# Kernel optimization log

Hardware: AMD Instinct MI355X
Metric: run time of the kernel (lower is better)

The kernel has to match this reference:

```python
import jax, jax.numpy as jnp
import numpy as np

H = 16       # num_attention_heads
KV = 4       # num_key_value_heads
HD = 128     # head_dim
BASE = 10000.0


def rotate_half(x):
    x1, x2 = jnp.split(x, 2, axis=-1)
    return jnp.concatenate((-x2, x1), axis=-1)


def rope_cos_sin(position_ids):
    # inv_freq: (HD/2,)
    inv_freq = 1.0 / (BASE ** (jnp.arange(0, HD, 2, dtype=jnp.float32) / HD))
    freqs = position_ids.astype(jnp.float32)[..., None] * inv_freq  # (B, S, HD/2)
    emb = jnp.concatenate((freqs, freqs), axis=-1)  # (B, S, HD)
    return jnp.cos(emb), jnp.sin(emb)


def setup_inputs() -> dict:
    key = jax.random.key(0)
    ks = jax.random.split(key, 5)
    B, S, D = 2, 2048, 2048
    sc = 1.0 / np.sqrt(D)
    return {
        "hidden_states": jax.random.normal(ks[0], (B, S, D), jnp.float32),
        "position_ids": jnp.broadcast_to(jnp.arange(S, dtype=jnp.int32), (B, S)),
        "wq": jax.random.normal(ks[1], (H * HD, D), jnp.float32) * sc,
        "wk": jax.random.normal(ks[2], (KV * HD, D), jnp.float32) * sc,
        "wv": jax.random.normal(ks[3], (KV * HD, D), jnp.float32) * sc,
        "wo": jax.random.normal(ks[4], (H * HD, H * HD), jnp.float32) * sc,
    }


def attention_forward(hidden_states, position_ids, wq, wk, wv, wo):
    B, S, D = hidden_states.shape
    n_rep = H // KV
    # projections -> (B, heads, S, HD)
    q = (hidden_states @ wq.T).reshape(B, S, H, HD).transpose(0, 2, 1, 3)
    k = (hidden_states @ wk.T).reshape(B, S, KV, HD).transpose(0, 2, 1, 3)
    v = (hidden_states @ wv.T).reshape(B, S, KV, HD).transpose(0, 2, 1, 3)
    # RoPE
    cos, sin = rope_cos_sin(position_ids)  # (B, S, HD)
    cos = cos[:, None]  # (B, 1, S, HD)
    sin = sin[:, None]
    q = q * cos + rotate_half(q) * sin
    k = k * cos + rotate_half(k) * sin
    # repeat kv heads for GQA: (B, KV, S, HD) -> (B, H, S, HD)
    k = jnp.repeat(k, n_rep, axis=1)
    v = jnp.repeat(v, n_rep, axis=1)
    scale = 1.0 / np.sqrt(HD)
    scores = jnp.einsum("bhqd,bhkd->bhqk", q, k) * scale
    attn = jax.nn.softmax(scores.astype(jnp.float32), axis=-1).astype(q.dtype)
    out = jnp.einsum("bhqk,bhkd->bhqd", attn, v)
    out = out.transpose(0, 2, 1, 3).reshape(B, S, H * HD)
    return out @ wo.T


def reference(hidden_states, position_ids, wq, wk, wv, wo):
    return attention_forward(hidden_states, position_ids, wq, wk, wv, wo)
```

## Files before the change

kernel.cpp:

```cpp
#include <hip/hip_runtime.h>
#include <hip/hip_bf16.h>
#include <math.h>


typedef __attribute__((ext_vector_type(4))) float f32x4;
typedef __attribute__((ext_vector_type(8))) short short8;
typedef __attribute__((ext_vector_type(4))) unsigned short u16x4;
typedef __attribute__((ext_vector_type(8))) unsigned short u16x8;

static __device__ __forceinline__ unsigned short f2bf(float x) {
    unsigned u = __builtin_bit_cast(unsigned, x);
    u += 0x7fffu + ((u >> 16) & 1u);
    return (unsigned short)(u >> 16);
}
static __device__ __forceinline__ float bf2f(unsigned short h) {
    unsigned u = ((unsigned)h) << 16;
    return __builtin_bit_cast(float, u);
}
static __device__ __forceinline__ float exp2_fast(float x) {
    float r;
    asm volatile("v_exp_f32 %0, %1" : "=v"(r) : "v"(x));
    return r;
}
static __device__ __forceinline__ void gload16(const unsigned short* g, unsigned short* lds) {
    __builtin_amdgcn_global_load_lds((const __attribute__((address_space(1))) void*)g,
                                     (__attribute__((address_space(3))) void*)lds, 16, 0, 0);
}

__global__ __launch_bounds__(256) void k_prep(const float* __restrict__ hs,
                                              const float* __restrict__ wq,
                                              const float* __restrict__ wk,
                                              const float* __restrict__ wv,
                                              const float* __restrict__ wo,
                                              const int* __restrict__ pos_ids,
                                              unsigned short* __restrict__ hsb,
                                              unsigned short* __restrict__ wqkvb,
                                              unsigned short* __restrict__ wob,
                                              float2* __restrict__ tb) {
    long idx = (long)blockIdx.x * 256 + threadIdx.x;
    if (idx < 2097152) {
        f32x4 v = ((const f32x4*)hs)[idx];
        u16x4 o;
        o.x = f2bf(v.x); o.y = f2bf(v.y); o.z = f2bf(v.z); o.w = f2bf(v.w);
        ((u16x4*)hsb)[idx] = o;
    } else if (idx < 3670016) {
        long i = idx - 2097152;
        long flat = i * 4;
        int row = (int)(flat >> 11);
        int col = (int)(flat & 2047);
        const float* src;
        if (row < 2560) {
            int base = row & 2047;
            int hh = base >> 7, ii = base & 127;
            int d = (ii >> 1) + ((ii & 1) << 6);
            src = (row < 2048 ? wq : wk) + (size_t)(hh * 128 + d) * 2048;
        } else {
            src = wv + (size_t)(row - 2560) * 2048;
        }
        f32x4 v = *(const f32x4*)(src + col);
        u16x4 o;
        o.x = f2bf(v.x); o.y = f2bf(v.y); o.z = f2bf(v.z); o.w = f2bf(v.w);
        *(u16x4*)(wqkvb + flat) = o;
    } else if (idx < 4718592) {
        long i = idx - 3670016;
        f32x4 v = ((const f32x4*)wo)[i];
        u16x4 o;
        o.x = f2bf(v.x); o.y = f2bf(v.y); o.z = f2bf(v.z); o.w = f2bf(v.w);
        ((u16x4*)wob)[i] = o;
    } else {
        long j = idx - 4718592;
        int r = (int)(j >> 6);
        int i = (int)(j & 63);
        float pos = (float)pos_ids[r];
        float powv = (float)pow(10000.0, (double)i / 64.0);
        float invf = 1.0f / powv;
        float arg  = pos * invf;
        double a = (double)arg;
        tb[(size_t)r * 64 + i] = make_float2((float)cos(a), (float)sin(a));
    }
}

template <int EPI>
__global__ __launch_bounds__(256) void k_gemm(const unsigned short* __restrict__ A,
                                              const unsigned short* __restrict__ W,
                                              float* __restrict__ Cf,
                                              unsigned short* __restrict__ qkvt,
                                              unsigned short* __restrict__ vtb,
                                              const float2* __restrict__ tb,
                                              int M, int N, int K) {
    __shared__ unsigned short As[2][4096];
    __shared__ unsigned short Ws[2][4096];
    const int tid = threadIdx.x;
    const int lane = tid & 63;
    const int w = tid >> 6;
    const int q = lane & 15, g = lane >> 4;
    const int wr = w >> 1, wc = w & 1;

    const int nwg = gridDim.x * gridDim.y;
    const int id = blockIdx.y * gridDim.x + blockIdx.x;
    const int swz_id = (id & 7) * (nwg >> 3) + (id >> 3);
    const int bx = swz_id % gridDim.x;
    const int by = swz_id / gridDim.x;
    const long mbase = (long)by * 128;
    const long nbase = (long)bx * 128;

    const unsigned short* gA[2];
    const unsigned short* gW[2];
    #pragma unroll
    for (int j = 0; j < 2; ++j) {
        int r = j * 64 + (tid >> 2);
        int slot = (tid & 3) ^ ((r >> 1) & 3);
        gA[j] = A + (size_t)(mbase + r) * K + slot * 8;
        gW[j] = W + (size_t)(nbase + r) * K + slot * 8;
    }
    const int sa = (g ^ ((q >> 1) & 3)) * 8;

    f32x4 acc[4][4];
    #pragma unroll
    for (int m = 0; m < 4; ++m)
        #pragma unroll
        for (int n = 0; n < 4; ++n) acc[m][n] = (f32x4){0.f, 0.f, 0.f, 0.f};

    auto STAGE = [&](int buf) {
        #pragma unroll
        for (int j = 0; j < 2; ++j) {
            gload16(gA[j], &As[buf][j * 2048 + w * 512]);
            gload16(gW[j], &Ws[buf][j * 2048 + w * 512]);
            gA[j] += 32; gW[j] += 32;
        }
    };

    const int nk = K >> 5;
    STAGE(0);
    int cur = 0;
    for (int t = 0; t < nk; ++t) {
        if (t) __builtin_amdgcn_s_barrier();
        if (t + 1 < nk) {
            STAGE(cur ^ 1);
            asm volatile("s_waitcnt vmcnt(4)" ::: "memory");
        } else {
            asm volatile("s_waitcnt vmcnt(0)" ::: "memory");
        }
        __builtin_amdgcn_s_barrier();

        short8 af[4], bfr[4];
        #pragma unroll
        for (int m = 0; m < 4; ++m) af[m] = *(const short8*)&As[cur][(wr * 64 + m * 16 + q) * 32 + sa];
        #pragma unroll
        for (int n = 0; n < 4; ++n) bfr[n] = *(const short8*)&Ws[cur][(wc * 64 + n * 16 + q) * 32 + sa];
        #pragma unroll
        for (int m = 0; m < 4; ++m)
            #pragma unroll
            for (int n = 0; n < 4; ++n)
                acc[m][n] = __builtin_amdgcn_mfma_f32_16x16x32_bf16(af[m], bfr[n], acc[m][n], 0, 0, 0);
        cur ^= 1;
    }

    if (EPI == 0) {
        #pragma unroll
        for (int m = 0; m < 4; ++m)
            #pragma unroll
            for (int n = 0; n < 4; ++n)
                #pragma unroll
                for (int rr = 0; rr < 4; ++rr) {
                    long row = mbase + wr * 64 + m * 16 + 4 * g + rr;
                    long col = nbase + wc * 64 + n * 16 + q;
                    Cf[row * N + col] = acc[m][n][rr];
                }
    } else {
        const int tile = bx;
        if (tile >= 20) {
            const int kv = tile - 20;
            #pragma unroll
            for (int m = 0; m < 4; ++m)
                #pragma unroll
                for (int n = 0; n < 4; ++n) {
                    int c = wc * 64 + n * 16 + q;
                    long r0 = mbase + wr * 64 + m * 16 + 4 * g;
                    int b = (int)(r0 >> 11), s0 = (int)(r0 & 2047);
                    u16x4 pk;
                    #pragma unroll
                    for (int rr = 0; rr < 4; ++rr) pk[rr] = f2bf(acc[m][n][rr]);
                    *(u16x4*)(vtb + (size_t)((b * 4 + kv) * 128 + c) * 2048 + s0) = pk;
                }
        } else {
            const float scale = (tile < 16) ? 0.12751744f : 1.0f;
            const float sgn = (q & 1) ? 1.f : -1.f;
            #pragma unroll
            for (int m = 0; m < 4; ++m)
                #pragma unroll
                for (int rr = 0; rr < 4; ++rr) {
                    long row = mbase + wr * 64 + m * 16 + 4 * g + rr;
                    #pragma unroll
                    for (int n = 0; n < 4; ++n) {
                        int c = wc * 64 + n * 16 + q;
                        float x = acc[m][n][rr];
                        float p = __shfl_xor(x, 1);
                        float2 cs = tb[row * 64 + (c >> 1)];
                        float y = (x * cs.x + sgn * (p * cs.y)) * scale;
                        int dorig = (c >> 1) + ((c & 1) << 6);
                        long col = (tile < 16) ? (tile * 128 + dorig)
                                               : (2048 + (tile - 16) * 128 + dorig);
                        qkvt[row * 3072 + col] = f2bf(y);
                    }
                }
        }
    }
}

__global__ __launch_bounds__(256, 2) void k_flash(const unsigned short* __restrict__ qkv,
                                                  const unsigned short* __restrict__ vt,
                                                  unsigned short* __restrict__ aout) {
    __shared__ unsigned short Ks[2][8192];
    __shared__ unsigned short Vs[2][8192];
    __shared__ unsigned short Plds[4][1152];
    const int wg = blockIdx.x;
    const int kvg = wg & 7;
    const int inner = wg >> 3;
    const int h_in = inner & 3;
    const int qt = inner >> 2;
    const int b = kvg >> 2, kvh = kvg & 3;
    const int h = kvh * 4 + h_in;
    const int tid = threadIdx.x;
    const int w = tid >> 6, lane = tid & 63;
    const int q = lane & 15, g = lane >> 4;
    const int qrow = qt * 128 + w * 32;

    short8 qf[2][4];
    #pragma unroll
    for (int u = 0; u < 2; ++u) {
        const unsigned short* Qp = qkv + (size_t)(b * 2048 + qrow + u * 16 + q) * 3072 + h * 128 + g * 8;
        #pragma unroll
        for (int t = 0; t < 4; ++t) qf[u][t] = *(const short8*)(Qp + t * 32);
    }

    const unsigned short* Kbase = qkv + (size_t)(b * 2048) * 3072 + 2048 + kvh * 128;
    const unsigned short* Vbase = vt + (size_t)((b * 4 + kvh) * 128) * 2048;
    const unsigned short* gK[4];
    const unsigned short* gV[4];
    #pragma unroll
    for (int i = 0; i < 4; ++i) {
        int rowK = w * 16 + i * 4 + (lane >> 4);
        gK[i] = Kbase + (size_t)rowK * 3072 + (((lane & 15) ^ (rowK & 7)) << 3);
        int rowV = w * 32 + i * 8 + (lane >> 3);
        gV[i] = Vbase + (size_t)rowV * 2048 + (((lane & 7) ^ (rowV & 7)) << 3);
    }

    const int swz = (q & 7) << 3;
    int tcK[4];
    #pragma unroll
    for (int t = 0; t < 4; ++t) tcK[t] = (t * 32 + g * 8) ^ swz;

    unsigned short* Pw = Plds[w];

    float m_run[2] = {-INFINITY, -INFINITY};
    float l_run[2] = {0.f, 0.f};
    f32x4 o[2][8];
    #pragma unroll
    for (int u = 0; u < 2; ++u)
        #pragma unroll
        for (int nf = 0; nf < 8; ++nf) o[u][nf] = (f32x4){0.f, 0.f, 0.f, 0.f};

    auto STAGE = [&](int buf) {
        #pragma unroll
        for (int i = 0; i < 4; ++i) {
            gload16(gK[i], &Ks[buf][w * 2048 + i * 512]);
            gload16(gV[i], &Vs[buf][w * 2048 + i * 512]);
            gK[i] += 64 * 3072;
            gV[i] += 64;
        }
    };

    STAGE(0);
    int cur = 0;
    for (int t0 = 0; t0 < 32; ++t0) {
        if (t0 > 0) __builtin_amdgcn_s_barrier();
        if (t0 + 1 < 32) {
            STAGE(cur ^ 1);
            asm volatile("s_waitcnt vmcnt(8)" ::: "memory");
        } else {
            asm volatile("s_waitcnt vmcnt(0)" ::: "memory");
        }
        __builtin_amdgcn_s_barrier();

        const unsigned short* Kt = Ks[cur];
        const unsigned short* Vt = Vs[cur];

        f32x4 st[2][4];
        #pragma unroll
        for (int ks = 0; ks < 4; ++ks) {
            f32x4 a0 = (f32x4){0.f, 0.f, 0.f, 0.f};
            f32x4 a1 = (f32x4){0.f, 0.f, 0.f, 0.f};
            int rb = (ks * 16 + q) * 128;
            #pragma unroll
            for (int t = 0; t < 4; ++t) {
                short8 kf = *(const short8*)&Kt[rb + tcK[t]];
                a0 = __builtin_amdgcn_mfma_f32_16x16x32_bf16(kf, qf[0][t], a0, 0, 0, 0);
                a1 = __builtin_amdgcn_mfma_f32_16x16x32_bf16(kf, qf[1][t], a1, 0, 0, 0);
            }
            st[0][ks] = a0; st[1][ks] = a1;
        }

        short8 vf[8][2];
        #pragma unroll
        for (int nf = 0; nf < 8; ++nf) {
            int rb = (nf * 16 + q) * 64;
            #pragma unroll
            for (int t = 0; t < 2; ++t) vf[nf][t] = *(const short8*)&Vt[rb + tcK[t]];
        }

        #pragma unroll
        for (int u = 0; u < 2; ++u) {
            float mx = fmaxf(
                fmaxf(fmaxf(fmaxf(st[u][0][0], st[u][0][1]), fmaxf(st[u][0][2], st[u][0][3])),
                      fmaxf(fmaxf(st[u][1][0], st[u][1][1]), fmaxf(st[u][1][2], st[u][1][3]))),
                fmaxf(fmaxf(fmaxf(st[u][2][0], st[u][2][1]), fmaxf(st[u][2][2], st[u][2][3])),
                      fmaxf(fmaxf(st[u][3][0], st[u][3][1]), fmaxf(st[u][3][2], st[u][3][3]))));
            mx = fmaxf(mx, __shfl_xor(mx, 16));
            mx = fmaxf(mx, __shfl_xor(mx, 32));
            if (__any(mx - m_run[u] > 8.0f)) {
                float mn = fmaxf(m_run[u], mx);
                float sc = exp2_fast(m_run[u] - mn);
                l_run[u] *= sc;
                f32x4 sv;
                #pragma unroll
                for (int rr = 0; rr < 4; ++rr) sv[rr] = __shfl(sc, 4 * g + rr);
                #pragma unroll
                for (int nf = 0; nf < 8; ++nf) o[u][nf] *= sv;
                m_run[u] = mn;
            }
            f32x4 pe[4];
            #pragma unroll
            for (int ks = 0; ks < 4; ++ks)
                #pragma unroll
                for (int rr = 0; rr < 4; ++rr) pe[ks][rr] = exp2_fast(st[u][ks][rr] - m_run[u]);
            f32x4 ls4 = (pe[0] + pe[1]) + (pe[2] + pe[3]);
            float ls = (ls4[0] + ls4[1]) + (ls4[2] + ls4[3]);
            ls += __shfl_xor(ls, 16);
            ls += __shfl_xor(ls, 32);
            l_run[u] += ls;

            #pragma unroll
            for (int ks = 0; ks < 4; ++ks) {
                u16x4 pk;
                #pragma unroll
                for (int rr = 0; rr < 4; ++rr) pk[rr] = f2bf(pe[ks][rr]);
                *(u16x4*)&Pw[q * 72 + ks * 16 + 4 * g] = pk;
            }
            asm volatile("s_waitcnt lgkmcnt(0)" ::: "memory");
            short8 pa0 = *(const short8*)&Pw[q * 72 + g * 8];
            short8 pa1 = *(const short8*)&Pw[q * 72 + 32 + g * 8];

            #pragma unroll
            for (int nf = 0; nf < 8; ++nf) {
                f32x4 a = o[u][nf];
                a = __builtin_amdgcn_mfma_f32_16x16x32_bf16(pa0, vf[nf][0], a, 0, 0, 0);
                a = __builtin_amdgcn_mfma_f32_16x16x32_bf16(pa1, vf[nf][1], a, 0, 0, 0);
                o[u][nf] = a;
            }
        }
        cur ^= 1;
    }

    #pragma unroll
    for (int u = 0; u < 2; ++u) {
        f32x4 li;
        #pragma unroll
        for (int rr = 0; rr < 4; ++rr) li[rr] = __shfl(l_run[u], 4 * g + rr);
        #pragma unroll
        for (int nf = 0; nf < 8; ++nf)
            #pragma unroll
            for (int rr = 0; rr < 4; ++rr) {
                size_t row = (size_t)(b * 2048 + qrow + u * 16 + 4 * g + rr);
                aout[row * 2048 + h * 128 + nf * 16 + q] = f2bf(o[u][nf][rr] / li[rr]);
            }
    }
}

extern "C" void kernel_launch(void* const* d_in, const int* in_sizes, int n_in,
                              void* d_out, int out_size, void* d_ws, size_t ws_size,
                              hipStream_t stream) {
    (void)in_sizes; (void)n_in; (void)out_size; (void)ws_size;
    const float* hs = (const float*)d_in[0];
    const int* pos  = (const int*)d_in[1];
    const float* wq = (const float*)d_in[2];
    const float* wk = (const float*)d_in[3];
    const float* wv = (const float*)d_in[4];
    const float* wo = (const float*)d_in[5];
    float* out = (float*)d_out;

    unsigned short* hsb   = (unsigned short*)d_ws;
    unsigned short* wqkvb = hsb + (size_t)4096 * 2048;
    unsigned short* wob   = wqkvb + (size_t)3072 * 2048;
    unsigned short* qkvt  = wob + (size_t)2048 * 2048;
    unsigned short* vtb   = qkvt + (size_t)4096 * 3072;
    float2* tb            = (float2*)(vtb + (size_t)8 * 128 * 2048);
    unsigned short* aoutb = (unsigned short*)(tb + (size_t)4096 * 64);

    k_prep<<<19456, 256, 0, stream>>>(hs, wq, wk, wv, wo, pos, hsb, wqkvb, wob, tb);
    k_gemm<1><<<dim3(24, 32), 256, 0, stream>>>(hsb, wqkvb, nullptr, qkvt, vtb, tb, 4096, 3072, 2048);
    k_flash<<<dim3(512), 256, 0, stream>>>(qkvt, vtb, aoutb);
    k_gemm<0><<<dim3(16, 32), 256, 0, stream>>>(aoutb, wob, out, nullptr, nullptr, nullptr, 4096, 2048, 2048);
}
```

Before: 226.5 us.

## Rewrite projection GEMMs with 8-wave 256-row tiles and phased K=64 pipelining

Replaces the 128x128, 4-wave GEMM with an 8-wave (512-thread) kernel. The QKV projection now uses 256x256 tiles and the output projection 256x128 tiles, with a K-step of 64 and an XOR-swizzled LDS layout. The main loop is split into phases that interleave global-to-LDS prefetch of the next tile with MFMA work on the current one, and raise wave priority around the MFMA blocks. The aim is more data reuse per LDS load and better overlap of memory with compute. The cost is more barriers, higher register and LDS pressure, and fewer workgroups (192 and 256) on a large-CU GPU, so occupancy and wave quantization may suffer.

```diff
diff --git a/kernel.cpp b/kernel.cpp
--- a/kernel.cpp
+++ b/kernel.cpp
@@ -12,10 +12,6 @@
     unsigned u = __builtin_bit_cast(unsigned, x);
     u += 0x7fffu + ((u >> 16) & 1u);
     return (unsigned short)(u >> 16);
-}
-static __device__ __forceinline__ float bf2f(unsigned short h) {
-    unsigned u = ((unsigned)h) << 16;
-    return __builtin_bit_cast(float, u);
 }
 static __device__ __forceinline__ float exp2_fast(float x) {
     float r;
@@ -81,130 +77,201 @@
 }
 
 template <int EPI>
-__global__ __launch_bounds__(256) void k_gemm(const unsigned short* __restrict__ A,
-                                              const unsigned short* __restrict__ W,
-                                              float* __restrict__ Cf,
-                                              unsigned short* __restrict__ qkvt,
-                                              unsigned short* __restrict__ vtb,
-                                              const float2* __restrict__ tb,
-                                              int M, int N, int K) {
-    __shared__ unsigned short As[2][4096];
-    __shared__ unsigned short Ws[2][4096];
+__global__ __launch_bounds__(512, 2) void k_gemm8(const unsigned short* __restrict__ A,
+                                                  const unsigned short* __restrict__ W,
+                                                  float* __restrict__ Cf,
+                                                  unsigned short* __restrict__ qkvt,
+                                                  unsigned short* __restrict__ vtb,
+                                                  const float2* __restrict__ tb,
+                                                  int M, int N, int K) {
+    constexpr int BN = EPI ? 256 : 128;
+    constexpr int BHALF = BN / 128;
+    __shared__ unsigned short As[2][16384];
+    __shared__ unsigned short Bs[2][BN * 64];
     const int tid = threadIdx.x;
     const int lane = tid & 63;
     const int w = tid >> 6;
     const int q = lane & 15, g = lane >> 4;
-    const int wr = w >> 1, wc = w & 1;
+    const int wr = w >> 2, wc = w & 3;
 
     const int nwg = gridDim.x * gridDim.y;
     const int id = blockIdx.y * gridDim.x + blockIdx.x;
     const int swz_id = (id & 7) * (nwg >> 3) + (id >> 3);
     const int bx = swz_id % gridDim.x;
     const int by = swz_id / gridDim.x;
-    const long mbase = (long)by * 128;
-    const long nbase = (long)bx * 128;
-
-    const unsigned short* gA[2];
-    const unsigned short* gW[2];
-    #pragma unroll
-    for (int j = 0; j < 2; ++j) {
-        int r = j * 64 + (tid >> 2);
-        int slot = (tid & 3) ^ ((r >> 1) & 3);
-        gA[j] = A + (size_t)(mbase + r) * K + slot * 8;
-        gW[j] = W + (size_t)(nbase + r) * K + slot * 8;
-    }
-    const int sa = (g ^ ((q >> 1) & 3)) * 8;
-
-    f32x4 acc[4][4];
-    #pragma unroll
-    for (int m = 0; m < 4; ++m)
-        #pragma unroll
-        for (int n = 0; n < 4; ++n) acc[m][n] = (f32x4){0.f, 0.f, 0.f, 0.f};
-
-    auto STAGE = [&](int buf) {
-        #pragma unroll
-        for (int j = 0; j < 2; ++j) {
-            gload16(gA[j], &As[buf][j * 2048 + w * 512]);
-            gload16(gW[j], &Ws[buf][j * 2048 + w * 512]);
-            gA[j] += 32; gW[j] += 32;
-        }
+    const long mbase = (long)by * 256;
+    const long nbase = (long)bx * BN;
+
+    const int lr = lane >> 3;
+    const int lslot = (lane & 7) ^ lr;
+    const unsigned short* pA[2][2];
+    const unsigned short* pB[BHALF][2];
+    #pragma unroll
+    for (int h = 0; h < 2; ++h)
+        #pragma unroll
+        for (int j = 0; j < 2; ++j)
+            pA[h][j] = A + (size_t)(mbase + h * 128 + w * 16 + j * 8 + lr) * K + lslot * 8;
+    #pragma unroll
+    for (int h = 0; h < BHALF; ++h)
+        #pragma unroll
+        for (int j = 0; j < 2; ++j)
+            pB[h][j] = W + (size_t)(nbase + h * 128 + w * 16 + j * 8 + lr) * K + lslot * 8;
+
+    auto ISSUE_A = [&](int buf, int h) {
+        gload16(pA[h][0], &As[buf][h * 8192 + w * 1024]);
+        gload16(pA[h][1], &As[buf][h * 8192 + w * 1024 + 512]);
+        pA[h][0] += 64; pA[h][1] += 64;
     };
-
-    const int nk = K >> 5;
-    STAGE(0);
-    int cur = 0;
-    for (int t = 0; t < nk; ++t) {
-        if (t) __builtin_amdgcn_s_barrier();
-        if (t + 1 < nk) {
-            STAGE(cur ^ 1);
-            asm volatile("s_waitcnt vmcnt(4)" ::: "memory");
-        } else {
-            asm volatile("s_waitcnt vmcnt(0)" ::: "memory");
-        }
-        __builtin_amdgcn_s_barrier();
-
-        short8 af[4], bfr[4];
-        #pragma unroll
-        for (int m = 0; m < 4; ++m) af[m] = *(const short8*)&As[cur][(wr * 64 + m * 16 + q) * 32 + sa];
-        #pragma unroll
-        for (int n = 0; n < 4; ++n) bfr[n] = *(const short8*)&Ws[cur][(wc * 64 + n * 16 + q) * 32 + sa];
-        #pragma unroll
-        for (int m = 0; m < 4; ++m)
-            #pragma unroll
-            for (int n = 0; n < 4; ++n)
-                acc[m][n] = __builtin_amdgcn_mfma_f32_16x16x32_bf16(af[m], bfr[n], acc[m][n], 0, 0, 0);
-        cur ^= 1;
-    }
-
-    if (EPI == 0) {
-        #pragma unroll
-        for (int m = 0; m < 4; ++m)
-            #pragma unroll
-            for (int n = 0; n < 4; ++n)
-                #pragma unroll
-                for (int rr = 0; rr < 4; ++rr) {
-                    long row = mbase + wr * 64 + m * 16 + 4 * g + rr;
-                    long col = nbase + wc * 64 + n * 16 + q;
-                    Cf[row * N + col] = acc[m][n][rr];
+    auto ISSUE_B = [&](int buf, int h) {
+        gload16(pB[h][0], &Bs[buf][h * 8192 + w * 1024]);
+        gload16(pB[h][1], &Bs[buf][h * 8192 + w * 1024 + 512]);
+        pB[h][0] += 64; pB[h][1] += 64;
+    };
+
+    const int xs = q & 7;
+    const int sl0 = (g ^ xs) * 8;
+    const int sl1 = ((4 + g) ^ xs) * 8;
+
+    const int NT = K >> 6;
+
+    if constexpr (EPI == 1) {
+        f32x4 acc[8][4];
+        #pragma unroll
+        for (int m = 0; m < 8; ++m)
+            #pragma unroll
+            for (int n = 0; n < 4; ++n) acc[m][n] = (f32x4){0.f, 0.f, 0.f, 0.f};
+        short8 a[4][2], bq[2][2];
+
+        auto loadA = [&](int cur, int mh) {
+            #pragma unroll
+            for (int mq = 0; mq < 4; ++mq) {
+                int r = (wr * 128 + mh * 64 + mq * 16 + q) * 64;
+                a[mq][0] = *(const short8*)&As[cur][r + sl0];
+                a[mq][1] = *(const short8*)&As[cur][r + sl1];
+            }
+        };
+        auto loadB = [&](int cur, int nh) {
+            #pragma unroll
+            for (int nq = 0; nq < 2; ++nq) {
+                int r = (wc * 64 + nh * 32 + nq * 16 + q) * 64;
+                bq[nq][0] = *(const short8*)&Bs[cur][r + sl0];
+                bq[nq][1] = *(const short8*)&Bs[cur][r + sl1];
+            }
+        };
+        auto mm = [&](int mh, int nh) {
+            __builtin_amdgcn_s_setprio(1);
+            #pragma unroll
+            for (int mq = 0; mq < 4; ++mq)
+                #pragma unroll
+                for (int nq = 0; nq < 2; ++nq) {
+                    f32x4 c = acc[mh * 4 + mq][nh * 2 + nq];
+                    c = __builtin_amdgcn_mfma_f32_16x16x32_bf16(a[mq][0], bq[nq][0], c, 0, 0, 0);
+                    c = __builtin_amdgcn_mfma_f32_16x16x32_bf16(a[mq][1], bq[nq][1], c, 0, 0, 0);
+                    acc[mh * 4 + mq][nh * 2 + nq] = c;
                 }
-    } else {
-        const int tile = bx;
-        if (tile >= 20) {
-            const int kv = tile - 20;
-            #pragma unroll
-            for (int m = 0; m < 4; ++m)
-                #pragma unroll
-                for (int n = 0; n < 4; ++n) {
-                    int c = wc * 64 + n * 16 + q;
-                    long r0 = mbase + wr * 64 + m * 16 + 4 * g;
-                    int b = (int)(r0 >> 11), s0 = (int)(r0 & 2047);
+            __builtin_amdgcn_s_setprio(0);
+        };
+
+        ISSUE_A(0, 0); ISSUE_A(0, 1); ISSUE_B(0, 0); ISSUE_B(0, 1);
+        for (int t = 0; t < NT; ++t) {
+            const int cur = t & 1, nxt = cur ^ 1;
+            const bool more = (t + 1 < NT);
+            if (more) { ISSUE_A(nxt, 0); asm volatile("s_waitcnt vmcnt(2)" ::: "memory"); }
+            else      { asm volatile("s_waitcnt vmcnt(0)" ::: "memory"); }
+            __builtin_amdgcn_s_barrier();
+            loadA(cur, 0); loadB(cur, 0); mm(0, 0);
+            __builtin_amdgcn_s_barrier();
+            if (more) ISSUE_A(nxt, 1);
+            loadA(cur, 1); mm(1, 0);
+            __builtin_amdgcn_s_barrier();
+            if (more) ISSUE_B(nxt, 0);
+            loadB(cur, 1); mm(1, 1);
+            __builtin_amdgcn_s_barrier();
+            if (more) ISSUE_B(nxt, 1);
+            loadA(cur, 0); mm(0, 1);
+            __builtin_amdgcn_s_barrier();
+        }
+
+        const float scale = (bx < 8) ? 0.12751744f : 1.0f;
+        const float sgn = (q & 1) ? 1.f : -1.f;
+        #pragma unroll
+        for (int m = 0; m < 8; ++m) {
+            long row0 = mbase + wr * 128 + m * 16 + 4 * g;
+            #pragma unroll
+            for (int n = 0; n < 4; ++n) {
+                int col256 = wc * 64 + n * 16 + q;
+                int hh = col256 >> 7, c = col256 & 127;
+                if (bx >= 10) {
+                    int kv = (bx - 10) * 2 + hh;
+                    int b = (int)(row0 >> 11), s0 = (int)(row0 & 2047);
                     u16x4 pk;
                     #pragma unroll
                     for (int rr = 0; rr < 4; ++rr) pk[rr] = f2bf(acc[m][n][rr]);
                     *(u16x4*)(vtb + (size_t)((b * 4 + kv) * 128 + c) * 2048 + s0) = pk;
-                }
-        } else {
-            const float scale = (tile < 16) ? 0.12751744f : 1.0f;
-            const float sgn = (q & 1) ? 1.f : -1.f;
-            #pragma unroll
-            for (int m = 0; m < 4; ++m)
-                #pragma unroll
-                for (int rr = 0; rr < 4; ++rr) {
-                    long row = mbase + wr * 64 + m * 16 + 4 * g + rr;
+                } else {
+                    int dorig = (c >> 1) + ((c & 1) << 6);
+                    long col = (bx < 8) ? (bx * 256 + hh * 128 + dorig)
+                                        : (2048 + (bx - 8) * 256 + hh * 128 + dorig);
                     #pragma unroll
-                    for (int n = 0; n < 4; ++n) {
-                        int c = wc * 64 + n * 16 + q;
+                    for (int rr = 0; rr < 4; ++rr) {
+                        long row = row0 + rr;
                         float x = acc[m][n][rr];
                         float p = __shfl_xor(x, 1);
                         float2 cs = tb[row * 64 + (c >> 1)];
                         float y = (x * cs.x + sgn * (p * cs.y)) * scale;
-                        int dorig = (c >> 1) + ((c & 1) << 6);
-                        long col = (tile < 16) ? (tile * 128 + dorig)
-                                               : (2048 + (tile - 16) * 128 + dorig);
                         qkvt[row * 3072 + col] = f2bf(y);
                     }
                 }
-        }
+            }
+        }
+    } else {
+        f32x4 acc[8][2];
+        #pragma unroll
+        for (int m = 0; m < 8; ++m)
+            #pragma unroll
+            for (int n = 0; n < 2; ++n) acc[m][n] = (f32x4){0.f, 0.f, 0.f, 0.f};
+        short8 a[8], bq[2];
+
+        auto phase = [&](int cur, int slx) {
+            #pragma unroll
+            for (int m = 0; m < 8; ++m)
+                a[m] = *(const short8*)&As[cur][(wr * 128 + m * 16 + q) * 64 + slx];
+            #pragma unroll
+            for (int n = 0; n < 2; ++n)
+                bq[n] = *(const short8*)&Bs[cur][(wc * 32 + n * 16 + q) * 64 + slx];
+            __builtin_amdgcn_s_setprio(1);
+            #pragma unroll
+            for (int m = 0; m < 8; ++m)
+                #pragma unroll
+                for (int n = 0; n < 2; ++n)
+                    acc[m][n] = __builtin_amdgcn_mfma_f32_16x16x32_bf16(a[m], bq[n], acc[m][n], 0, 0, 0);
+            __builtin_amdgcn_s_setprio(0);
+        };
+
+        ISSUE_A(0, 0); ISSUE_A(0, 1); ISSUE_B(0, 0);
+        for (int t = 0; t < NT; ++t) {
+            const int cur = t & 1, nxt = cur ^ 1;
+            const bool more = (t + 1 < NT);
+            if (more) { ISSUE_A(nxt, 0); asm volatile("s_waitcnt vmcnt(2)" ::: "memory"); }
+            else      { asm volatile("s_waitcnt vmcnt(0)" ::: "memory"); }
+            __builtin_amdgcn_s_barrier();
+            phase(cur, sl0);
+            __builtin_amdgcn_s_barrier();
+            if (more) { ISSUE_A(nxt, 1); ISSUE_B(nxt, 0); }
+            phase(cur, sl1);
+            __builtin_amdgcn_s_barrier();
+        }
+
+        #pragma unroll
+        for (int m = 0; m < 8; ++m)
+            #pragma unroll
+            for (int n = 0; n < 2; ++n)
+                #pragma unroll
+                for (int rr = 0; rr < 4; ++rr) {
+                    long row = mbase + wr * 128 + m * 16 + 4 * g + rr;
+                    long col = nbase + wc * 32 + n * 16 + q;
+                    Cf[row * N + col] = acc[m][n][rr];
+                }
     }
 }
 
@@ -398,7 +465,7 @@
     unsigned short* aoutb = (unsigned short*)(tb + (size_t)4096 * 64);
 
     k_prep<<<19456, 256, 0, stream>>>(hs, wq, wk, wv, wo, pos, hsb, wqkvb, wob, tb);
-    k_gemm<1><<<dim3(24, 32), 256, 0, stream>>>(hsb, wqkvb, nullptr, qkvt, vtb, tb, 4096, 3072, 2048);
+    k_gemm8<1><<<dim3(12, 16), 512, 0, stream>>>(hsb, wqkvb, nullptr, qkvt, vtb, tb, 4096, 3072, 2048);
     k_flash<<<dim3(512), 256, 0, stream>>>(qkvt, vtb, aoutb);
-    k_gemm<0><<<dim3(16, 32), 256, 0, stream>>>(aoutb, wob, out, nullptr, nullptr, nullptr, 4096, 2048, 2048);
-}
+    k_gemm8<0><<<dim3(16, 16), 512, 0, stream>>>(aoutb, wob, out, nullptr, nullptr, nullptr, 4096, 2048, 2048);
+}
```

Measured after the change: 266.7 us. 17.7% more time.

## Halve flash-attention query and KV tiles to double workgroup count

Applied to the files above, without the earlier changes.

Each flash workgroup now handles 64 query rows instead of 128, with 16 rows per wave, and streams K/V in 32-key tiles instead of 64. The grid doubles to 1024 workgroups, LDS per block shrinks, and launch bounds ask for 3 blocks per CU, so occupancy and load balance across the CUs should improve. In exchange, each K/V tile is reused by half as many query rows, so global/L2 traffic per query doubles, and the loop runs twice as many iterations with barriers. The final normalization now multiplies by a reciprocal instead of dividing.

```diff
diff --git a/kernel.cpp b/kernel.cpp
--- a/kernel.cpp
+++ b/kernel.cpp
@@ -12,10 +12,6 @@
     unsigned u = __builtin_bit_cast(unsigned, x);
     u += 0x7fffu + ((u >> 16) & 1u);
     return (unsigned short)(u >> 16);
-}
-static __device__ __forceinline__ float bf2f(unsigned short h) {
-    unsigned u = ((unsigned)h) << 16;
-    return __builtin_bit_cast(float, u);
 }
 static __device__ __forceinline__ float exp2_fast(float x) {
     float r;
@@ -208,12 +204,12 @@
     }
 }
 
-__global__ __launch_bounds__(256, 2) void k_flash(const unsigned short* __restrict__ qkv,
+__global__ __launch_bounds__(256, 3) void k_flash(const unsigned short* __restrict__ qkv,
                                                   const unsigned short* __restrict__ vt,
                                                   unsigned short* __restrict__ aout) {
-    __shared__ unsigned short Ks[2][8192];
-    __shared__ unsigned short Vs[2][8192];
-    __shared__ unsigned short Plds[4][1152];
+    __shared__ unsigned short Ks[2][4096];
+    __shared__ unsigned short Vs[2][4096];
+    __shared__ unsigned short Plds[4][640];
     const int wg = blockIdx.x;
     const int kvg = wg & 7;
     const int inner = wg >> 3;
@@ -224,60 +220,57 @@
     const int tid = threadIdx.x;
     const int w = tid >> 6, lane = tid & 63;
     const int q = lane & 15, g = lane >> 4;
-    const int qrow = qt * 128 + w * 32;
-
-    short8 qf[2][4];
-    #pragma unroll
-    for (int u = 0; u < 2; ++u) {
-        const unsigned short* Qp = qkv + (size_t)(b * 2048 + qrow + u * 16 + q) * 3072 + h * 128 + g * 8;
-        #pragma unroll
-        for (int t = 0; t < 4; ++t) qf[u][t] = *(const short8*)(Qp + t * 32);
+    const int qrow = qt * 64 + w * 16;
+
+    short8 qf[4];
+    {
+        const unsigned short* Qp = qkv + (size_t)(b * 2048 + qrow + q) * 3072 + h * 128 + g * 8;
+        #pragma unroll
+        for (int t = 0; t < 4; ++t) qf[t] = *(const short8*)(Qp + t * 32);
     }
 
     const unsigned short* Kbase = qkv + (size_t)(b * 2048) * 3072 + 2048 + kvh * 128;
     const unsigned short* Vbase = vt + (size_t)((b * 4 + kvh) * 128) * 2048;
-    const unsigned short* gK[4];
-    const unsigned short* gV[4];
-    #pragma unroll
-    for (int i = 0; i < 4; ++i) {
-        int rowK = w * 16 + i * 4 + (lane >> 4);
-        gK[i] = Kbase + (size_t)rowK * 3072 + (((lane & 15) ^ (rowK & 7)) << 3);
-        int rowV = w * 32 + i * 8 + (lane >> 3);
-        gV[i] = Vbase + (size_t)rowV * 2048 + (((lane & 7) ^ (rowV & 7)) << 3);
+    const unsigned short* gK[2];
+    const unsigned short* gV[2];
+    #pragma unroll
+    for (int j = 0; j < 2; ++j) {
+        int rK = j * 16 + (tid >> 4);
+        gK[j] = Kbase + (size_t)rK * 3072 + (((tid & 15) ^ (rK & 7)) << 3);
+        int rV = j * 64 + (tid >> 2);
+        gV[j] = Vbase + (size_t)rV * 2048 + (((tid & 3) ^ (rV & 3)) << 3);
     }
 
     const int swz = (q & 7) << 3;
     int tcK[4];
     #pragma unroll
     for (int t = 0; t < 4; ++t) tcK[t] = (t * 32 + g * 8) ^ swz;
+    const int tcV = (g ^ (q & 3)) * 8;
 
     unsigned short* Pw = Plds[w];
 
-    float m_run[2] = {-INFINITY, -INFINITY};
-    float l_run[2] = {0.f, 0.f};
-    f32x4 o[2][8];
-    #pragma unroll
-    for (int u = 0; u < 2; ++u)
-        #pragma unroll
-        for (int nf = 0; nf < 8; ++nf) o[u][nf] = (f32x4){0.f, 0.f, 0.f, 0.f};
+    float m_run = -INFINITY, l_run = 0.f;
+    f32x4 o[8];
+    #pragma unroll
+    for (int nf = 0; nf < 8; ++nf) o[nf] = (f32x4){0.f, 0.f, 0.f, 0.f};
 
     auto STAGE = [&](int buf) {
         #pragma unroll
-        for (int i = 0; i < 4; ++i) {
-            gload16(gK[i], &Ks[buf][w * 2048 + i * 512]);
-            gload16(gV[i], &Vs[buf][w * 2048 + i * 512]);
-            gK[i] += 64 * 3072;
-            gV[i] += 64;
+        for (int j = 0; j < 2; ++j) {
+            gload16(gK[j], &Ks[buf][j * 2048 + w * 512]);
+            gload16(gV[j], &Vs[buf][j * 2048 + w * 512]);
+            gK[j] += 32 * 3072;
+            gV[j] += 32;
         }
     };
 
     STAGE(0);
     int cur = 0;
-    for (int t0 = 0; t0 < 32; ++t0) {
+    for (int t0 = 0; t0 < 64; ++t0) {
         if (t0 > 0) __builtin_amdgcn_s_barrier();
-        if (t0 + 1 < 32) {
+        if (t0 + 1 < 64) {
             STAGE(cur ^ 1);
-            asm volatile("s_waitcnt vmcnt(8)" ::: "memory");
+            asm volatile("s_waitcnt vmcnt(4)" ::: "memory");
         } else {
             asm volatile("s_waitcnt vmcnt(0)" ::: "memory");
         }
@@ -286,95 +279,79 @@
         const unsigned short* Kt = Ks[cur];
         const unsigned short* Vt = Vs[cur];
 
-        f32x4 st[2][4];
-        #pragma unroll
-        for (int ks = 0; ks < 4; ++ks) {
-            f32x4 a0 = (f32x4){0.f, 0.f, 0.f, 0.f};
-            f32x4 a1 = (f32x4){0.f, 0.f, 0.f, 0.f};
+        f32x4 st[2];
+        #pragma unroll
+        for (int ks = 0; ks < 2; ++ks) {
+            f32x4 a = (f32x4){0.f, 0.f, 0.f, 0.f};
             int rb = (ks * 16 + q) * 128;
             #pragma unroll
             for (int t = 0; t < 4; ++t) {
                 short8 kf = *(const short8*)&Kt[rb + tcK[t]];
-                a0 = __builtin_amdgcn_mfma_f32_16x16x32_bf16(kf, qf[0][t], a0, 0, 0, 0);
-                a1 = __builtin_amdgcn_mfma_f32_16x16x32_bf16(kf, qf[1][t], a1, 0, 0, 0);
+                a = __builtin_amdgcn_mfma_f32_16x16x32_bf16(kf, qf[t], a, 0, 0, 0);
             }
-            st[0][ks] = a0; st[1][ks] = a1;
-        }
-
-        short8 vf[8][2];
-        #pragma unroll
-        for (int nf = 0; nf < 8; ++nf) {
-            int rb = (nf * 16 + q) * 64;
-            #pragma unroll
-            for (int t = 0; t < 2; ++t) vf[nf][t] = *(const short8*)&Vt[rb + tcK[t]];
-        }
-
-        #pragma unroll
-        for (int u = 0; u < 2; ++u) {
-            float mx = fmaxf(
-                fmaxf(fmaxf(fmaxf(st[u][0][0], st[u][0][1]), fmaxf(st[u][0][2], st[u][0][3])),
-                      fmaxf(fmaxf(st[u][1][0], st[u][1][1]), fmaxf(st[u][1][2], st[u][1][3]))),
-                fmaxf(fmaxf(fmaxf(st[u][2][0], st[u][2][1]), fmaxf(st[u][2][2], st[u][2][3])),
-                      fmaxf(fmaxf(st[u][3][0], st[u][3][1]), fmaxf(st[u][3][2], st[u][3][3]))));
-            mx = fmaxf(mx, __shfl_xor(mx, 16));
-            mx = fmaxf(mx, __shfl_xor(mx, 32));
-            if (__any(mx - m_run[u] > 8.0f)) {
-                float mn = fmaxf(m_run[u], mx);
-                float sc = exp2_fast(m_run[u] - mn);
-                l_run[u] *= sc;
-                f32x4 sv;
-                #pragma unroll
-                for (int rr = 0; rr < 4; ++rr) sv[rr] = __shfl(sc, 4 * g + rr);
-                #pragma unroll
-                for (int nf = 0; nf < 8; ++nf) o[u][nf] *= sv;
-                m_run[u] = mn;
-            }
-            f32x4 pe[4];
-            #pragma unroll
-            for (int ks = 0; ks < 4; ++ks)
-                #pragma unroll
-                for (int rr = 0; rr < 4; ++rr) pe[ks][rr] = exp2_fast(st[u][ks][rr] - m_run[u]);
-            f32x4 ls4 = (pe[0] + pe[1]) + (pe[2] + pe[3]);
-            float ls = (ls4[0] + ls4[1]) + (ls4[2] + ls4[3]);
-            ls += __shfl_xor(ls, 16);
-            ls += __shfl_xor(ls, 32);
-            l_run[u] += ls;
-
-            #pragma unroll
-            for (int ks = 0; ks < 4; ++ks) {
-                u16x4 pk;
-                #pragma unroll
-                for (int rr = 0; rr < 4; ++rr) pk[rr] = f2bf(pe[ks][rr]);
-                *(u16x4*)&Pw[q * 72 + ks * 16 + 4 * g] = pk;
-            }
-            asm volatile("s_waitcnt lgkmcnt(0)" ::: "memory");
-            short8 pa0 = *(const short8*)&Pw[q * 72 + g * 8];
-            short8 pa1 = *(const short8*)&Pw[q * 72 + 32 + g * 8];
-
-            #pragma unroll
-            for (int nf = 0; nf < 8; ++nf) {
-                f32x4 a = o[u][nf];
-                a = __builtin_amdgcn_mfma_f32_16x16x32_bf16(pa0, vf[nf][0], a, 0, 0, 0);
-                a = __builtin_amdgcn_mfma_f32_16x16x32_bf16(pa1, vf[nf][1], a, 0, 0, 0);
-                o[u][nf] = a;
-            }
-        }
+            st[ks] = a;
+        }
+
+        short8 vf[8];
+        #pragma unroll
+        for (int nf = 0; nf < 8; ++nf)
+            vf[nf] = *(const short8*)&Vt[(nf * 16 + q) * 32 + tcV];
+
+        float mx = fmaxf(fmaxf(fmaxf(st[0][0], st[0][1]), fmaxf(st[0][2], st[0][3])),
+                         fmaxf(fmaxf(st[1][0], st[1][1]), fmaxf(st[1][2], st[1][3])));
+        mx = fmaxf(mx, __shfl_xor(mx, 16));
+        mx = fmaxf(mx, __shfl_xor(mx, 32));
+        if (__any(mx - m_run > 8.0f)) {
+            float mn = fmaxf(m_run, mx);
+            float sc = exp2_fast(m_run - mn);
+            l_run *= sc;
+            f32x4 sv;
+            #pragma unroll
+            for (int rr = 0; rr < 4; ++rr) sv[rr] = __shfl(sc, 4 * g + rr);
+            #pragma unroll
+            for (int nf = 0; nf < 8; ++nf) o[nf] *= sv;
+            m_run = mn;
+        }
+        f32x4 pe[2];
+        #pragma unroll
+        for (int ks = 0; ks < 2; ++ks)
+            #pragma unroll
+            for (int rr = 0; rr < 4; ++rr) pe[ks][rr] = exp2_fast(st[ks][rr] - m_run);
+        f32x4 ls4 = pe[0] + pe[1];
+        float ls = (ls4[0] + ls4[1]) + (ls4[2] + ls4[3]);
+        ls += __shfl_xor(ls, 16);
+        ls += __shfl_xor(ls, 32);
+        l_run += ls;
+
+        #pragma unroll
+        for (int ks = 0; ks < 2; ++ks) {
+            u16x4 pk;
+            #pragma unroll
+            for (int rr = 0; rr < 4; ++rr) pk[rr] = f2bf(pe[ks][rr]);
+            *(u16x4*)&Pw[q * 40 + ks * 16 + 4 * g] = pk;
+        }
+        asm volatile("s_waitcnt lgkmcnt(0)" ::: "memory");
+        short8 pa = *(const short8*)&Pw[q * 40 + g * 8];
+
+        #pragma unroll
+        for (int nf = 0; nf < 8; ++nf)
+            o[nf] = __builtin_amdgcn_mfma_f32_16x16x32_bf16(pa, vf[nf], o[nf], 0, 0, 0);
+
         cur ^= 1;
     }
 
-    #pragma unroll
-    for (int u = 0; u < 2; ++u) {
-        f32x4 li;
-        #pragma unroll
-        for (int rr = 0; rr < 4; ++rr) li[rr] = __shfl(l_run[u], 4 * g + rr);
-        #pragma unroll
-        for (int nf = 0; nf < 8; ++nf)
-            #pragma unroll
-            for (int rr = 0; rr < 4; ++rr) {
-                size_t row = (size_t)(b * 2048 + qrow + u * 16 + 4 * g + rr);
-                aout[row * 2048 + h * 128 + nf * 16 + q] = f2bf(o[u][nf][rr] / li[rr]);
-            }
-    }
+    f32x4 li;
+    #pragma unroll
+    for (int rr = 0; rr < 4; ++rr) li[rr] = __shfl(l_run, 4 * g + rr);
+    #pragma unroll
+    for (int rr = 0; rr < 4; ++rr) li[rr] = 1.0f / li[rr];
+    #pragma unroll
+    for (int nf = 0; nf < 8; ++nf)
+        #pragma unroll
+        for (int rr = 0; rr < 4; ++rr) {
+            size_t row = (size_t)(b * 2048 + qrow + 4 * g + rr);
+            aout[row * 2048 + h * 128 + nf * 16 + q] = f2bf(o[nf][rr] * li[rr]);
+        }
 }
 
 extern "C" void kernel_launch(void* const* d_in, const int* in_sizes, int n_in,
@@ -399,6 +376,6 @@
 
     k_prep<<<19456, 256, 0, stream>>>(hs, wq, wk, wv, wo, pos, hsb, wqkvb, wob, tb);
     k_gemm<1><<<dim3(24, 32), 256, 0, stream>>>(hsb, wqkvb, nullptr, qkvt, vtb, tb, 4096, 3072, 2048);
-    k_flash<<<dim3(512), 256, 0, stream>>>(qkvt, vtb, aoutb);
+    k_flash<<<dim3(1024), 256, 0, stream>>>(qkvt, vtb, aoutb);
     k_gemm<0><<<dim3(16, 32), 256, 0, stream>>>(aoutb, wob, out, nullptr, nullptr, nullptr, 4096, 2048, 2048);
 }
```

New measurement: 255.7 us. 12.9% more time.
